# Optimization experiments

Measured on AMD Instinct MI355X. Metric: run time of the kernel, lower is better.

## Reference

```python
import jax, jax.numpy as jnp
import numpy as np

WS = 14           # window_size
N = WS * WS       # tokens = 196
DIM = 768
H = 12
HD = DIM // H     # 64
B = 256
KSZ = 3


def make_local_mask():
    # True = masked out; 3x3 neighborhood around each query is kept (False)
    mask = np.ones((N, N), dtype=bool)
    for i in range(WS):
        for j in range(WS):
            cur = np.ones((WS, WS), dtype=bool)
            stx, sty = max(i - KSZ // 2, 0), max(j - KSZ // 2, 0)
            edx, edy = min(i + KSZ // 2, WS - 1), min(j + KSZ // 2, WS - 1)
            cur[stx:edx + 1, sty:edy + 1] = False
            mask[i * WS + j] = cur.reshape(-1)
    return mask


def make_rel_idx():
    coords = np.stack(np.meshgrid(np.arange(WS), np.arange(WS), indexing='ij'))  # [2,WS,WS]
    flat = coords.reshape(2, -1)                                                  # [2,N]
    rel = flat[:, :, None] - flat[:, None, :]                                     # [2,N,N]
    rel = rel.transpose(1, 2, 0).astype(np.int32)                                 # [N,N,2]
    rel[:, :, 0] += WS - 1
    rel[:, :, 1] += WS - 1
    rel[:, :, 0] *= 2 * WS - 1
    return rel.sum(-1)                                                            # [N,N] in [0, (2WS-1)^2)


def setup_inputs() -> dict:
    key = jax.random.key(0)
    ks = jax.random.split(key, 5)
    return {
        'x': jax.random.normal(ks[0], (B, N, DIM), jnp.float32),
        'w_qkv': jax.random.normal(ks[1], (3 * DIM, DIM), jnp.float32) * 0.02,
        'rpb_table': jax.random.normal(ks[2], ((2 * WS - 1) ** 2, H), jnp.float32) * 0.02,
        'proj_w': jax.random.normal(ks[3], (DIM, DIM), jnp.float32) * 0.02,
        'proj_b': jax.random.normal(ks[4], (DIM,), jnp.float32) * 0.02,
        'mask': jnp.asarray(make_local_mask()),
        'rel_idx': jnp.asarray(make_rel_idx()),
    }


def reference(x, w_qkv, rpb_table, proj_w, proj_b, mask, rel_idx):
    b, n, c = x.shape
    scale = HD ** -0.5
    qkv = x @ w_qkv.T                                   # [B,N,3*DIM]
    qkv = qkv.reshape(b, n, 3, H, HD).transpose(2, 0, 3, 1, 4)  # [3,B,H,N,HD]
    q, k, v = qkv[0] * scale, qkv[1], qkv[2]
    attn = jnp.einsum('bhqd,bhkd->bhqk', q, k)          # [B,H,N,N]
    neg = -jnp.finfo(attn.dtype).max
    attn = jnp.where(mask, neg, attn)
    # relative position bias gather: [N,N] indices into [T,H] -> [H,N,N]
    rpb = rpb_table[rel_idx].transpose(2, 0, 1)
    attn = attn + rpb[None]
    attn = jax.nn.softmax(attn, axis=-1)
    out = jnp.einsum('bhqk,bhkd->bhqd', attn, v)        # [B,H,N,HD]
    out = out.transpose(0, 2, 1, 3).reshape(b, n, H * HD)
    return out @ proj_w.T + proj_b
```

## Files before the change

### kernel.cpp

```cpp
#include <hip/hip_runtime.h>
#include <cstdint>
#include <cstddef>

typedef unsigned short u16;
typedef __attribute__((ext_vector_type(8))) short bf16x8;
typedef __attribute__((ext_vector_type(4))) float f32x4;

__device__ __forceinline__ u16 f2bf(float f) {
    unsigned u = __float_as_uint(f);
    u += 0x7FFF + ((u >> 16) & 1);
    return (u16)(u >> 16);
}

__global__ __launch_bounds__(256) void cvt_bf16(const float4* __restrict__ in,
                                                u16* __restrict__ out, int n4) {
    int i = blockIdx.x * 256 + threadIdx.x;
    if (i >= n4) return;
    float4 v = in[i];
    ushort4 o;
    o.x = f2bf(v.x); o.y = f2bf(v.y); o.z = f2bf(v.z); o.w = f2bf(v.w);
    ((ushort4*)out)[i] = o;
}

__device__ __forceinline__ void gl_lds16(const u16* g, u16* l) {
    __builtin_amdgcn_global_load_lds(
        (const __attribute__((address_space(1))) void*)g,
        (__attribute__((address_space(3))) void*)l, 16, 0, 0);
}

#define MFMA16(a, b, c) __builtin_amdgcn_mfma_f32_16x16x32_bf16(a, b, c, 0, 0, 0)

__device__ __forceinline__ void BARRIER() {
    asm volatile("" ::: "memory");
    __builtin_amdgcn_s_barrier();
    asm volatile("" ::: "memory");
}
#define LGKM0() asm volatile("s_waitcnt lgkmcnt(0)" ::: "memory")

__device__ __forceinline__ bf16x8 lds_frag(const u16* base, int r, int c) {
    return *(const bf16x8*)((const char*)base + (r << 7) + ((c ^ (r & 7)) << 4));
}

__device__ __forceinline__ void stage_half(const u16* gbase, int K, u16* lbase,
                                           int kt, int h, int srow, int wuoff)
{
    const u16* gp = gbase + (size_t)(h * 128 + srow) * K + kt * 64;
    char* lp = (char*)lbase + h * 16384 + wuoff;
    gl_lds16(gp, (u16*)lp);
    gl_lds16(gp + (size_t)64 * K, (u16*)(lp + 8192));
}

__device__ __forceinline__ void stage_tile(const u16* Ag, const u16* Bg, int K,
                                           u16* Ab, u16* Bb, int kt,
                                           int srow, int wuoff)
{
    stage_half(Ag, K, Ab, kt, 0, srow, wuoff);
    stage_half(Ag, K, Ab, kt, 1, srow, wuoff);
    stage_half(Bg, K, Bb, kt, 0, srow, wuoff);
    stage_half(Bg, K, Bb, kt, 1, srow, wuoff);
}

template <bool IS_QKV>
__global__ __launch_bounds__(512, 2)
void gemm256(const u16* __restrict__ A, const u16* __restrict__ Bt,
             const float* __restrict__ bias, void* __restrict__ Cout,
             int M, int N, int K)
{
    __shared__ u16 As[2][16384];
    __shared__ u16 Bs[2][16384];

    const int tid = threadIdx.x;
    const int w   = tid >> 6;
    const int l   = tid & 63;
    const int wr  = w >> 2;
    const int wc  = w & 3;
    const int fr  = l & 15;
    const int ck0 = l >> 4;

    const int gx = gridDim.x;
    const int nwg = gx * gridDim.y;
    const int orig = blockIdx.y * gx + blockIdx.x;
    const int qq = nwg >> 3, rr = nwg & 7;
    const int xcd = orig & 7, idx = orig >> 3;
    const int wg = (xcd < rr) ? (xcd * (qq + 1) + idx)
                              : (rr * (qq + 1) + (xcd - rr) * qq + idx);
    const int bx = wg % gx, by = wg / gx;
    const int m0 = by * 256, n0 = bx * 256;

    const int srow   = w * 8 + (l >> 3);
    const int schunk = ((l & 7) ^ (l >> 3)) * 8;
    const int wuoff  = w * 1024;

    const u16* Ag = A  + (size_t)m0 * K + schunk;
    const u16* Bg = Bt + (size_t)n0 * K + schunk;

    f32x4 acc[8][4] = {};
    const int NT = K >> 6;

    stage_tile(Ag, Bg, K, As[0], Bs[0], 0, srow, wuoff);
    stage_tile(Ag, Bg, K, As[1], Bs[1], 1, srow, wuoff);
    asm volatile("s_waitcnt vmcnt(8)" ::: "memory");
    BARRIER();

    for (int g = 0; g < NT; ++g) {
        const u16* Ab = As[g & 1];
        const u16* Bb = Bs[g & 1];
        u16* Acu = As[g & 1];
        u16* Bcu = Bs[g & 1];

        bf16x8 a0[8], a1[8], b0[4], b1[4];

        #pragma unroll
        for (int mi = 0; mi < 8; ++mi) a0[mi] = lds_frag(Ab, wr * 128 + mi * 16 + fr, ck0);
        b0[0] = lds_frag(Bb, wc * 64 + 0 * 16 + fr, ck0);
        b0[1] = lds_frag(Bb, wc * 64 + 1 * 16 + fr, ck0);
        BARRIER();
        LGKM0();
        __builtin_amdgcn_s_setprio(1);
        #pragma unroll
        for (int mi = 0; mi < 8; ++mi) {
            acc[mi][0] = MFMA16(a0[mi], b0[0], acc[mi][0]);
            acc[mi][1] = MFMA16(a0[mi], b0[1], acc[mi][1]);
        }
        __builtin_amdgcn_s_setprio(0);
        BARRIER();

        b0[2] = lds_frag(Bb, wc * 64 + 2 * 16 + fr, ck0);
        b0[3] = lds_frag(Bb, wc * 64 + 3 * 16 + fr, ck0);
        #pragma unroll
        for (int mi = 0; mi < 8; ++mi) a1[mi] = lds_frag(Ab, wr * 128 + mi * 16 + fr, ck0 + 4);
        #pragma unroll
        for (int ni = 0; ni < 4; ++ni) b1[ni] = lds_frag(Bb, wc * 64 + ni * 16 + fr, ck0 + 4);
        BARRIER();
        LGKM0();
        __builtin_amdgcn_s_setprio(1);
        #pragma unroll
        for (int mi = 0; mi < 8; ++mi) {
            acc[mi][2] = MFMA16(a0[mi], b0[2], acc[mi][2]);
            acc[mi][3] = MFMA16(a0[mi], b0[3], acc[mi][3]);
        }
        __builtin_amdgcn_s_setprio(0);
        BARRIER();

        if (g + 2 < NT) stage_tile(Ag, Bg, K, Acu, Bcu, g + 2, srow, wuoff);
        BARRIER();
        __builtin_amdgcn_s_setprio(1);
        #pragma unroll
        for (int mi = 0; mi < 8; ++mi) {
            acc[mi][0] = MFMA16(a1[mi], b1[0], acc[mi][0]);
            acc[mi][1] = MFMA16(a1[mi], b1[1], acc[mi][1]);
        }
        __builtin_amdgcn_s_setprio(0);
        BARRIER();

        __builtin_amdgcn_s_setprio(1);
        #pragma unroll
        for (int mi = 0; mi < 8; ++mi) {
            acc[mi][2] = MFMA16(a1[mi], b1[2], acc[mi][2]);
            acc[mi][3] = MFMA16(a1[mi], b1[3], acc[mi][3]);
        }
        __builtin_amdgcn_s_setprio(0);
        if (g < NT - 2) { asm volatile("s_waitcnt vmcnt(8)" ::: "memory"); }
        else            { asm volatile("s_waitcnt vmcnt(0)" ::: "memory"); }
        BARRIER();
    }

    if (IS_QKV) {
        u16* C = (u16*)Cout;
        #pragma unroll
        for (int mi = 0; mi < 8; ++mi) {
            const int r0 = m0 + wr * 128 + mi * 16 + (l >> 4) * 4;
            #pragma unroll
            for (int ni = 0; ni < 4; ++ni) {
                const int col = n0 + wc * 64 + ni * 16 + fr;
                const float sc = (col < 768) ? 0.125f : 1.0f;
                #pragma unroll
                for (int r = 0; r < 4; ++r)
                    C[(size_t)(r0 + r) * N + col] = f2bf(acc[mi][ni][r] * sc);
            }
        }
    } else {
        float* C = (float*)Cout;
        #pragma unroll
        for (int mi = 0; mi < 8; ++mi) {
            const int r0 = m0 + wr * 128 + mi * 16 + (l >> 4) * 4;
            #pragma unroll
            for (int ni = 0; ni < 4; ++ni) {
                const int col = n0 + wc * 64 + ni * 16 + fr;
                const float b = bias[col];
                #pragma unroll
                for (int r = 0; r < 4; ++r)
                    C[(size_t)(r0 + r) * N + col] = acc[mi][ni][r] + b;
            }
        }
    }
}

__device__ __forceinline__ void unpack8(uint4 d, float* f) {
    f[0] = __uint_as_float(d.x << 16); f[1] = __uint_as_float(d.x & 0xFFFF0000u);
    f[2] = __uint_as_float(d.y << 16); f[3] = __uint_as_float(d.y & 0xFFFF0000u);
    f[4] = __uint_as_float(d.z << 16); f[5] = __uint_as_float(d.z & 0xFFFF0000u);
    f[6] = __uint_as_float(d.w << 16); f[7] = __uint_as_float(d.w & 0xFFFF0000u);
}

__global__ __launch_bounds__(256)
void attn_lds(const u16* __restrict__ qkv, const float* __restrict__ rpb,
              u16* __restrict__ out)
{
    __shared__ u16 Ks[196 * 64];
    __shared__ u16 Vs[196 * 64];

    const int tid = threadIdx.x;
    const int bh  = blockIdx.x;
    const int b   = bh / 12;
    const int h   = bh - b * 12;
    const size_t base = (size_t)b * 196 * 2304 + h * 64;

    for (int c = tid; c < 1568; c += 256) {
        const int t = c >> 3, s = c & 7;
        const u16* kg = qkv + base + (size_t)t * 2304 + 768 + s * 8;
        uint4 kd = *(const uint4*)kg;
        uint4 vd = *(const uint4*)(kg + 768);
        const int off = t * 64 + ((s * 8) ^ ((t & 7) << 3));
        *(uint4*)&Ks[off] = kd;
        *(uint4*)&Vs[off] = vd;
    }

    float rpb9[9];
    #pragma unroll
    for (int a = 0; a < 9; ++a) {
        const int di = a / 3 - 1, dj = a % 3 - 1;
        rpb9[a] = rpb[((13 - di) * 27 + (13 - dj)) * 12 + h];
    }

    __syncthreads();

    const int w   = tid >> 6;
    const int sub = (tid >> 3) & 7;
    const int sl  = tid & 7;

    for (int p = 0; p < 7; ++p) {
        const int t = p * 32 + w * 8 + sub;
        const bool qv = t < 196;
        const int tt = qv ? t : 195;
        const int i = tt / 14, j = tt % 14;

        float qf[8];
        unpack8(*(const uint4*)(qkv + base + (size_t)tt * 2304 + sl * 8), qf);

        float s[9];
        int   t2a[9];
        #pragma unroll
        for (int a = 0; a < 9; ++a) {
            const int di = a / 3 - 1, dj = a % 3 - 1;
            const int i2 = i + di, j2 = j + dj;
            const bool valid = ((unsigned)i2 < 14u) && ((unsigned)j2 < 14u);
            const int t2 = valid ? (i2 * 14 + j2) : tt;
            t2a[a] = t2;
            float kf[8];
            unpack8(*(const uint4*)&Ks[t2 * 64 + ((sl * 8) ^ ((t2 & 7) << 3))], kf);
            float pp = qf[0] * kf[0];
            #pragma unroll
            for (int d = 1; d < 8; ++d) pp = fmaf(qf[d], kf[d], pp);
            pp += __shfl_xor(pp, 1);
            pp += __shfl_xor(pp, 2);
            pp += __shfl_xor(pp, 4);
            s[a] = valid ? (pp + rpb9[a]) : -1e30f;
        }
        float mx = s[0];
        #pragma unroll
        for (int a = 1; a < 9; ++a) mx = fmaxf(mx, s[a]);

        float den = 0.f, o[8] = {};
        #pragma unroll
        for (int a = 0; a < 9; ++a) {
            float vf[8];
            const int t2 = t2a[a];
            unpack8(*(const uint4*)&Vs[t2 * 64 + ((sl * 8) ^ ((t2 & 7) << 3))], vf);
            const float pe = __expf(s[a] - mx);
            den += pe;
            #pragma unroll
            for (int d = 0; d < 8; ++d) o[d] = fmaf(pe, vf[d], o[d]);
        }
        const float r = 1.0f / den;
        if (qv) {
            ushort4 o0, o1;
            o0.x = f2bf(o[0] * r); o0.y = f2bf(o[1] * r);
            o0.z = f2bf(o[2] * r); o0.w = f2bf(o[3] * r);
            o1.x = f2bf(o[4] * r); o1.y = f2bf(o[5] * r);
            o1.z = f2bf(o[6] * r); o1.w = f2bf(o[7] * r);
            u16* op = out + (size_t)(b * 196 + t) * 768 + h * 64 + sl * 8;
            *(ushort4*)op = o0;
            *(ushort4*)(op + 4) = o1;
        }
    }
}

extern "C" void kernel_launch(void* const* d_in, const int* in_sizes, int n_in,
                              void* d_out, int out_size, void* d_ws, size_t ws_size,
                              hipStream_t stream)
{
    const float* x      = (const float*)d_in[0];
    const float* w_qkv  = (const float*)d_in[1];
    const float* rpb    = (const float*)d_in[2];
    const float* proj_w = (const float*)d_in[3];
    const float* proj_b = (const float*)d_in[4];
    float* out = (float*)d_out;

    char* ws = (char*)d_ws;
    u16* x_bf    = (u16*)(ws);
    u16* wqkv_bf = (u16*)(ws + 77070336ULL);
    u16* pw_bf   = (u16*)(ws + 80609280ULL);
    u16* qkv_bf  = (u16*)(ws + 81788928ULL);
    u16* attn_bf = (u16*)(ws + 312999936ULL);

    cvt_bf16<<<37632, 256, 0, stream>>>((const float4*)x,      x_bf,    9633792);
    cvt_bf16<<<1728,  256, 0, stream>>>((const float4*)w_qkv,  wqkv_bf, 442368);
    cvt_bf16<<<576,   256, 0, stream>>>((const float4*)proj_w, pw_bf,   147456);

    gemm256<true><<<dim3(9, 196), 512, 0, stream>>>(
        x_bf, wqkv_bf, nullptr, qkv_bf, 50176, 2304, 768);

    attn_lds<<<3072, 256, 0, stream>>>(qkv_bf, rpb, attn_bf);

    gemm256<false><<<dim3(3, 196), 512, 0, stream>>>(
        attn_bf, pw_bf, proj_b, out, 50176, 768, 768);
}
```

Baseline: 686.9 us.

## Fuse bf16 conversions, interleave GEMM half-tile prefetch, read V from global in attention

The three fp32-to-bf16 conversion launches are merged into one kernel that picks its source by thread index, saving two launches. The GEMM main loop now issues its global-to-LDS half-tile loads spread across the four MFMA phases instead of as one burst, with a matching vmcnt wait, to smooth memory traffic under compute. The attention kernel stops staging V in LDS and reads V rows straight from global (L2), halving its shared memory to raise occupancy, at the cost of uncoalesced scattered global loads. The half-tile staging also changes buffer-reuse timing, which risks LDS write-after-read hazards.

```diff
diff --git a/kernel.cpp b/kernel.cpp
--- a/kernel.cpp
+++ b/kernel.cpp
@@ -12,14 +12,21 @@
     return (u16)(u >> 16);
 }
 
-__global__ __launch_bounds__(256) void cvt_bf16(const float4* __restrict__ in,
-                                                u16* __restrict__ out, int n4) {
+__global__ __launch_bounds__(256)
+void cvt3(const float4* __restrict__ a, u16* __restrict__ oa, int na4,
+          const float4* __restrict__ b, u16* __restrict__ ob, int nb4,
+          const float4* __restrict__ c, u16* __restrict__ oc, int nc4)
+{
     int i = blockIdx.x * 256 + threadIdx.x;
-    if (i >= n4) return;
-    float4 v = in[i];
+    const float4* src; u16* dst; int idx;
+    if (i < na4)                    { src = a; dst = oa; idx = i; }
+    else if (i < na4 + nb4)         { src = b; dst = ob; idx = i - na4; }
+    else if (i < na4 + nb4 + nc4)   { src = c; dst = oc; idx = i - na4 - nb4; }
+    else return;
+    float4 v = src[idx];
     ushort4 o;
     o.x = f2bf(v.x); o.y = f2bf(v.y); o.z = f2bf(v.z); o.w = f2bf(v.w);
-    ((ushort4*)out)[i] = o;
+    ((ushort4*)dst)[idx] = o;
 }
 
 __device__ __forceinline__ void gl_lds16(const u16* g, u16* l) {
@@ -48,16 +55,6 @@
     char* lp = (char*)lbase + h * 16384 + wuoff;
     gl_lds16(gp, (u16*)lp);
     gl_lds16(gp + (size_t)64 * K, (u16*)(lp + 8192));
-}
-
-__device__ __forceinline__ void stage_tile(const u16* Ag, const u16* Bg, int K,
-                                           u16* Ab, u16* Bb, int kt,
-                                           int srow, int wuoff)
-{
-    stage_half(Ag, K, Ab, kt, 0, srow, wuoff);
-    stage_half(Ag, K, Ab, kt, 1, srow, wuoff);
-    stage_half(Bg, K, Bb, kt, 0, srow, wuoff);
-    stage_half(Bg, K, Bb, kt, 1, srow, wuoff);
 }
 
 template <bool IS_QKV>
@@ -97,14 +94,20 @@
     f32x4 acc[8][4] = {};
     const int NT = K >> 6;
 
-    stage_tile(Ag, Bg, K, As[0], Bs[0], 0, srow, wuoff);
-    stage_tile(Ag, Bg, K, As[1], Bs[1], 1, srow, wuoff);
-    asm volatile("s_waitcnt vmcnt(8)" ::: "memory");
+    stage_half(Ag, K, As[0], 0, 0, srow, wuoff);
+    stage_half(Bg, K, Bs[0], 0, 0, srow, wuoff);
+    stage_half(Ag, K, As[0], 0, 1, srow, wuoff);
+    stage_half(Bg, K, Bs[0], 0, 1, srow, wuoff);
+    stage_half(Ag, K, As[1], 1, 0, srow, wuoff);
+    stage_half(Bg, K, Bs[1], 1, 0, srow, wuoff);
+    asm volatile("s_waitcnt vmcnt(4)" ::: "memory");
     BARRIER();
 
     for (int g = 0; g < NT; ++g) {
         const u16* Ab = As[g & 1];
         const u16* Bb = Bs[g & 1];
+        u16* Anx = As[(g + 1) & 1];
+        u16* Bnx = Bs[(g + 1) & 1];
         u16* Acu = As[g & 1];
         u16* Bcu = Bs[g & 1];
 
@@ -114,6 +117,7 @@
         for (int mi = 0; mi < 8; ++mi) a0[mi] = lds_frag(Ab, wr * 128 + mi * 16 + fr, ck0);
         b0[0] = lds_frag(Bb, wc * 64 + 0 * 16 + fr, ck0);
         b0[1] = lds_frag(Bb, wc * 64 + 1 * 16 + fr, ck0);
+        if (g + 1 < NT) stage_half(Ag, K, Anx, g + 1, 1, srow, wuoff);
         BARRIER();
         LGKM0();
         __builtin_amdgcn_s_setprio(1);
@@ -131,6 +135,7 @@
         for (int mi = 0; mi < 8; ++mi) a1[mi] = lds_frag(Ab, wr * 128 + mi * 16 + fr, ck0 + 4);
         #pragma unroll
         for (int ni = 0; ni < 4; ++ni) b1[ni] = lds_frag(Bb, wc * 64 + ni * 16 + fr, ck0 + 4);
+        if (g + 1 < NT) stage_half(Bg, K, Bnx, g + 1, 1, srow, wuoff);
         BARRIER();
         LGKM0();
         __builtin_amdgcn_s_setprio(1);
@@ -142,7 +147,7 @@
         __builtin_amdgcn_s_setprio(0);
         BARRIER();
 
-        if (g + 2 < NT) stage_tile(Ag, Bg, K, Acu, Bcu, g + 2, srow, wuoff);
+        if (g + 2 < NT) stage_half(Ag, K, Acu, g + 2, 0, srow, wuoff);
         BARRIER();
         __builtin_amdgcn_s_setprio(1);
         #pragma unroll
@@ -153,6 +158,7 @@
         __builtin_amdgcn_s_setprio(0);
         BARRIER();
 
+        if (g + 2 < NT) stage_half(Bg, K, Bcu, g + 2, 0, srow, wuoff);
         __builtin_amdgcn_s_setprio(1);
         #pragma unroll
         for (int mi = 0; mi < 8; ++mi) {
@@ -160,7 +166,7 @@
             acc[mi][3] = MFMA16(a1[mi], b1[3], acc[mi][3]);
         }
         __builtin_amdgcn_s_setprio(0);
-        if (g < NT - 2) { asm volatile("s_waitcnt vmcnt(8)" ::: "memory"); }
+        if (g < NT - 2) { asm volatile("s_waitcnt vmcnt(4)" ::: "memory"); }
         else            { asm volatile("s_waitcnt vmcnt(0)" ::: "memory"); }
         BARRIER();
     }
@@ -204,11 +210,10 @@
 }
 
 __global__ __launch_bounds__(256)
-void attn_lds(const u16* __restrict__ qkv, const float* __restrict__ rpb,
-              u16* __restrict__ out)
+void attn_k_lds(const u16* __restrict__ qkv, const float* __restrict__ rpb,
+                u16* __restrict__ out)
 {
     __shared__ u16 Ks[196 * 64];
-    __shared__ u16 Vs[196 * 64];
 
     const int tid = threadIdx.x;
     const int bh  = blockIdx.x;
@@ -218,12 +223,8 @@
 
     for (int c = tid; c < 1568; c += 256) {
         const int t = c >> 3, s = c & 7;
-        const u16* kg = qkv + base + (size_t)t * 2304 + 768 + s * 8;
-        uint4 kd = *(const uint4*)kg;
-        uint4 vd = *(const uint4*)(kg + 768);
-        const int off = t * 64 + ((s * 8) ^ ((t & 7) << 3));
-        *(uint4*)&Ks[off] = kd;
-        *(uint4*)&Vs[off] = vd;
+        uint4 kd = *(const uint4*)(qkv + base + (size_t)t * 2304 + 768 + s * 8);
+        *(uint4*)&Ks[t * 64 + ((s * 8) ^ ((t & 7) << 3))] = kd;
     }
 
     float rpb9[9];
@@ -275,8 +276,7 @@
         #pragma unroll
         for (int a = 0; a < 9; ++a) {
             float vf[8];
-            const int t2 = t2a[a];
-            unpack8(*(const uint4*)&Vs[t2 * 64 + ((sl * 8) ^ ((t2 & 7) << 3))], vf);
+            unpack8(*(const uint4*)(qkv + base + (size_t)t2a[a] * 2304 + 1536 + sl * 8), vf);
             const float pe = __expf(s[a] - mx);
             den += pe;
             #pragma unroll
@@ -314,14 +314,14 @@
     u16* qkv_bf  = (u16*)(ws + 81788928ULL);
     u16* attn_bf = (u16*)(ws + 312999936ULL);
 
-    cvt_bf16<<<37632, 256, 0, stream>>>((const float4*)x,      x_bf,    9633792);
-    cvt_bf16<<<1728,  256, 0, stream>>>((const float4*)w_qkv,  wqkv_bf, 442368);
-    cvt_bf16<<<576,   256, 0, stream>>>((const float4*)proj_w, pw_bf,   147456);
+    cvt3<<<39936, 256, 0, stream>>>((const float4*)x,      x_bf,    9633792,
+                                    (const float4*)w_qkv,  wqkv_bf, 442368,
+                                    (const float4*)proj_w, pw_bf,   147456);
 
     gemm256<true><<<dim3(9, 196), 512, 0, stream>>>(
         x_bf, wqkv_bf, nullptr, qkv_bf, 50176, 2304, 768);
 
-    attn_lds<<<3072, 256, 0, stream>>>(qkv_bf, rpb, attn_bf);
+    attn_k_lds<<<3072, 256, 0, stream>>>(qkv_bf, rpb, attn_bf);
 
     gemm256<false><<<dim3(3, 196), 512, 0, stream>>>(
         attn_bf, pw_bf, proj_b, out, 50176, 768, 768);
```

After: 654.2 us. 1.05x faster.
